# Performance work log

Measured on AMD Instinct MI355X. Metric: run time of the kernel, lower is better.

The kernel has to match this reference:

```python
import jax, jax.numpy as jnp
import numpy as np

DT = 0.01          # integration timestep
TH_HI = 1.0        # upper firing threshold
TH_LO = -1.0       # lower firing threshold


def setup_inputs() -> dict:
    key = jax.random.key(0)
    inputs = jax.random.normal(key, (64, 256, 1024), dtype=jnp.float32)
    return {"inputs": inputs}


def reference(inputs):
    # inputs: [B, T, D] pre-activation drive at each timestep
    rates = jnp.tanh(inputs)                     # activation(inputs), [B, T, D]
    x = jnp.swapaxes(rates, 0, 1)                # [T, B, D] for scan over time

    def step(v, r):
        v = v + r * DT                           # integrate
        sp = (v >= TH_HI).astype(v.dtype)        # positive spike
        sn = (v <= TH_LO).astype(v.dtype)        # negative spike
        v = v - sp * TH_HI - sn * TH_LO          # subtractive (self-regulating) reset
        out = (sp - sn) / DT                     # signed spike train scaled by 1/dt
        return v, out

    v0 = jnp.zeros(x.shape[1:], dtype=x.dtype)   # initial membrane state
    _, spikes = jax.lax.scan(step, v0, x)        # spikes: [T, B, D]
    spikes = jnp.swapaxes(spikes, 0, 1)          # [B, T, D]

    # spiking-aware (straight-through) output: spikes forward, rates gradient
    out = rates + jax.lax.stop_gradient(spikes - rates)
    return out
```

## Files before the change

kernel.cpp:

```cpp
#include <hip/hip_runtime.h>

#define B_DIM 64
#define T_STEPS 256
#define D_DIM 1024
#define UNROLL 16

#define USE_FMA_POLY 1

__device__ __forceinline__ float xla_tanhf(float x) {
    const float kClamp = 7.90531110763549805f;
    float xc = fminf(fmaxf(x, -kClamp), kClamp);
    float x2 = xc * xc;
#if USE_FMA_POLY
    float p = __builtin_fmaf(x2, -2.76076847742355e-16f, 2.00018790482477e-13f);
    p = __builtin_fmaf(x2, p, -8.60467152213735e-11f);
    p = __builtin_fmaf(x2, p, 5.12229709037114e-08f);
    p = __builtin_fmaf(x2, p, 1.48572235717979e-05f);
    p = __builtin_fmaf(x2, p, 6.37261928875436e-04f);
    p = __builtin_fmaf(x2, p, 4.89352455891786e-03f);
    p = xc * p;
    float q = __builtin_fmaf(x2, 1.19825839466702e-06f, 1.18534705686654e-04f);
    q = __builtin_fmaf(x2, q, 2.26843463243900e-03f);
    q = __builtin_fmaf(x2, q, 4.89352518554385e-03f);
#else
    float p = __fadd_rn(__fmul_rn(x2, -2.76076847742355e-16f), 2.00018790482477e-13f);
    p = __fadd_rn(__fmul_rn(x2, p), -8.60467152213735e-11f);
    p = __fadd_rn(__fmul_rn(x2, p), 5.12229709037114e-08f);
    p = __fadd_rn(__fmul_rn(x2, p), 1.48572235717979e-05f);
    p = __fadd_rn(__fmul_rn(x2, p), 6.37261928875436e-04f);
    p = __fadd_rn(__fmul_rn(x2, p), 4.89352455891786e-03f);
    p = __fmul_rn(xc, p);
    float q = __fadd_rn(__fmul_rn(x2, 1.19825839466702e-06f), 1.18534705686654e-04f);
    q = __fadd_rn(__fmul_rn(x2, q), 2.26843463243900e-03f);
    q = __fadd_rn(__fmul_rn(x2, q), 4.89352518554385e-03f);
#endif
    float r = p / q;
    return (fabsf(x) < 0.0004f) ? x : r;
}

__global__ __launch_bounds__(256)
void spike_scan_kernel(const float* __restrict__ in, float* __restrict__ out) {
    const int gid = blockIdx.x * blockDim.x + threadIdx.x;
    const int b = gid >> 10;
    const int d = gid & (D_DIM - 1);
    const long base = (long)b * (T_STEPS * D_DIM) + d;
    const float* ip = in + base;
    float* op = out + base;

    float v = 0.0f;
    float x[UNROLL], xn[UNROLL];

    #pragma unroll
    for (int u = 0; u < UNROLL; ++u) x[u] = ip[u * D_DIM];

    constexpr int CHUNKS = T_STEPS / UNROLL;
    for (int c = 0; c < CHUNKS; ++c) {
        const float* ipc = ip + (c + 1) * UNROLL * D_DIM;
        float* opc = op + c * UNROLL * D_DIM;

        if (c + 1 < CHUNKS) {
            #pragma unroll
            for (int u = 0; u < UNROLL; ++u) xn[u] = ipc[u * D_DIM];
        }

        #pragma unroll
        for (int u = 0; u < UNROLL; ++u) {
            float r = xla_tanhf(x[u]);
#if USE_FMA_POLY
            v = __builtin_fmaf(r, 0.01f, v);
#else
            v = __fadd_rn(v, __fmul_rn(r, 0.01f));
#endif
            float sp = (v >= 1.0f)  ? 1.0f : 0.0f;
            float sn = (v <= -1.0f) ? 1.0f : 0.0f;
            v = (v - sp) + sn;
            opc[u * D_DIM] = (sp - sn) * 100.0f;
        }

        #pragma unroll
        for (int u = 0; u < UNROLL; ++u) x[u] = xn[u];
    }
}

extern "C" void kernel_launch(void* const* d_in, const int* in_sizes, int n_in,
                              void* d_out, int out_size, void* d_ws, size_t ws_size,
                              hipStream_t stream) {
    const float* in = (const float*)d_in[0];
    float* out = (float*)d_out;
    const int total = B_DIM * D_DIM;
    dim3 block(256);
    dim3 grid(total / 256);
    spike_scan_kernel<<<grid, block, 0, stream>>>(in, out);
}
```

Measured before the change: 124.0 us.

## Stage input chunks into LDS via async global_load_lds double buffering

Replaces per-thread register prefetch with asynchronous direct global-to-LDS loads of 32-timestep chunks into a double-buffered shared tile, with each wave loading rows of 256 floats. Output stores become nontemporal to avoid polluting the cache. The aim is to keep more bytes in flight and hide load latency on a grid of only 256 blocks. It adds a barrier per chunk and 64KB of LDS per block. The correctness of the sync depends on __syncthreads also waiting for the async LDS loads.

```diff
diff --git a/kernel.cpp b/kernel.cpp
--- a/kernel.cpp
+++ b/kernel.cpp
@@ -3,15 +3,17 @@
 #define B_DIM 64
 #define T_STEPS 256
 #define D_DIM 1024
-#define UNROLL 16
+#define CT 32
+#define CHUNKS (T_STEPS / CT)
+#define TPB 256
 
-#define USE_FMA_POLY 1
+typedef __attribute__((address_space(3))) void lds_void;
+typedef __attribute__((address_space(1))) const void glob_void;
 
 __device__ __forceinline__ float xla_tanhf(float x) {
     const float kClamp = 7.90531110763549805f;
     float xc = fminf(fmaxf(x, -kClamp), kClamp);
     float x2 = xc * xc;
-#if USE_FMA_POLY
     float p = __builtin_fmaf(x2, -2.76076847742355e-16f, 2.00018790482477e-13f);
     p = __builtin_fmaf(x2, p, -8.60467152213735e-11f);
     p = __builtin_fmaf(x2, p, 5.12229709037114e-08f);
@@ -22,63 +24,54 @@
     float q = __builtin_fmaf(x2, 1.19825839466702e-06f, 1.18534705686654e-04f);
     q = __builtin_fmaf(x2, q, 2.26843463243900e-03f);
     q = __builtin_fmaf(x2, q, 4.89352518554385e-03f);
-#else
-    float p = __fadd_rn(__fmul_rn(x2, -2.76076847742355e-16f), 2.00018790482477e-13f);
-    p = __fadd_rn(__fmul_rn(x2, p), -8.60467152213735e-11f);
-    p = __fadd_rn(__fmul_rn(x2, p), 5.12229709037114e-08f);
-    p = __fadd_rn(__fmul_rn(x2, p), 1.48572235717979e-05f);
-    p = __fadd_rn(__fmul_rn(x2, p), 6.37261928875436e-04f);
-    p = __fadd_rn(__fmul_rn(x2, p), 4.89352455891786e-03f);
-    p = __fmul_rn(xc, p);
-    float q = __fadd_rn(__fmul_rn(x2, 1.19825839466702e-06f), 1.18534705686654e-04f);
-    q = __fadd_rn(__fmul_rn(x2, q), 2.26843463243900e-03f);
-    q = __fadd_rn(__fmul_rn(x2, q), 4.89352518554385e-03f);
-#endif
     float r = p / q;
     return (fabsf(x) < 0.0004f) ? x : r;
 }
 
-__global__ __launch_bounds__(256)
+__global__ __launch_bounds__(TPB, 1)
 void spike_scan_kernel(const float* __restrict__ in, float* __restrict__ out) {
-    const int gid = blockIdx.x * blockDim.x + threadIdx.x;
-    const int b = gid >> 10;
-    const int d = gid & (D_DIM - 1);
-    const long base = (long)b * (T_STEPS * D_DIM) + d;
+    __shared__ float buf[2][CT][TPB];
+
+    const int tid = threadIdx.x;
+    const int blk = blockIdx.x;
+    const int b   = blk >> 2;
+    const int d0  = (blk & 3) << 8;
+    const size_t base = (size_t)b * (T_STEPS * D_DIM) + d0;
     const float* ip = in + base;
-    float* op = out + base;
+    float* op = out + base + tid;
 
+    const int wave = tid >> 6;
+    const int lane = tid & 63;
+
+    auto stage = [&](int c, int pp) {
+        const float* g0 = ip + (size_t)(c * CT + wave * 8) * D_DIM + lane * 4;
+        #pragma unroll
+        for (int r = 0; r < 8; ++r) {
+            __builtin_amdgcn_global_load_lds(
+                (glob_void*)(g0 + (size_t)r * D_DIM),
+                (lds_void*)&buf[pp][wave * 8 + r][0],
+                16, 0, 0);
+        }
+    };
+
+    stage(0, 0);
     float v = 0.0f;
-    float x[UNROLL], xn[UNROLL];
 
-    #pragma unroll
-    for (int u = 0; u < UNROLL; ++u) x[u] = ip[u * D_DIM];
+    for (int c = 0; c < CHUNKS; ++c) {
+        const int pp = c & 1;
+        __syncthreads();
+        if (c + 1 < CHUNKS) stage(c + 1, pp ^ 1);
 
-    constexpr int CHUNKS = T_STEPS / UNROLL;
-    for (int c = 0; c < CHUNKS; ++c) {
-        const float* ipc = ip + (c + 1) * UNROLL * D_DIM;
-        float* opc = op + c * UNROLL * D_DIM;
-
-        if (c + 1 < CHUNKS) {
-            #pragma unroll
-            for (int u = 0; u < UNROLL; ++u) xn[u] = ipc[u * D_DIM];
-        }
-
+        float* opc = op + (size_t)c * CT * D_DIM;
         #pragma unroll
-        for (int u = 0; u < UNROLL; ++u) {
-            float r = xla_tanhf(x[u]);
-#if USE_FMA_POLY
+        for (int u = 0; u < CT; ++u) {
+            float r = xla_tanhf(buf[pp][u][tid]);
             v = __builtin_fmaf(r, 0.01f, v);
-#else
-            v = __fadd_rn(v, __fmul_rn(r, 0.01f));
-#endif
             float sp = (v >= 1.0f)  ? 1.0f : 0.0f;
             float sn = (v <= -1.0f) ? 1.0f : 0.0f;
             v = (v - sp) + sn;
-            opc[u * D_DIM] = (sp - sn) * 100.0f;
+            __builtin_nontemporal_store((sp - sn) * 100.0f, opc + (size_t)u * D_DIM);
         }
-
-        #pragma unroll
-        for (int u = 0; u < UNROLL; ++u) x[u] = xn[u];
     }
 }
 
@@ -87,8 +80,7 @@
                               hipStream_t stream) {
     const float* in = (const float*)d_in[0];
     float* out = (float*)d_out;
-    const int total = B_DIM * D_DIM;
-    dim3 block(256);
-    dim3 grid(total / 256);
+    dim3 block(TPB);
+    dim3 grid(B_DIM * (D_DIM / TPB));
     spike_scan_kernel<<<grid, block, 0, stream>>>(in, out);
 }
```

Result: faster. 115.2 us (-7.1%).
